# Kernel tuning notes

Hardware: AMD Instinct MI355X
Metric: run time of the kernel (lower is better)

## Reference

```python
import jax, jax.numpy as jnp
import numpy as np

EPS = 1e-5  # nn.RMSNorm eps


def setup_inputs() -> dict:
    key = jax.random.key(0)
    ks = jax.random.split(key, 8)
    B, L, D, R = 4, 4096, 2048, 4
    return {
        "h": jax.random.normal(ks[0], (B, L, D), jnp.float32),
        "h_o": jax.random.normal(ks[1], (B, L, D), jnp.float32),
        "static_alpha": jax.random.normal(ks[2], (R, R + 1), jnp.float32),
        "static_beta": jax.random.normal(ks[3], (R,), jnp.float32),
        "dynamic_alpha_fn": jax.random.normal(ks[4], (D, R + 1), jnp.float32) * 0.02,
        "dynamic_alpha_scale": jax.random.uniform(ks[5], (1,), jnp.float32, 0.005, 0.02),
        "dynamic_beta_fn": jax.random.normal(ks[6], (D,), jnp.float32) * 0.02,
        "dynamic_beta_scale": jnp.array([0.01], jnp.float32),
        "rms_weight": jax.random.uniform(ks[7], (D,), jnp.float32, 0.5, 1.5),
    }


def reference(h, h_o, static_alpha, static_beta, dynamic_alpha_fn,
              dynamic_alpha_scale, dynamic_beta_fn, dynamic_beta_scale,
              rms_weight):
    # RMSNorm over last dim with learnable weight (dynamic branch only)
    h_norm = h * jax.lax.rsqrt(jnp.mean(h * h, axis=-1, keepdims=True) + EPS) * rms_weight

    # dynamic alpha: [B,L,rate+1] offset broadcast against static [rate,rate+1]
    alpha_offset = jnp.tanh(h_norm @ dynamic_alpha_fn) * dynamic_alpha_scale  # [B,L,R+1]
    alpha = alpha_offset[:, :, None, :] + static_alpha                        # [B,L,R,R+1]

    # dynamic beta: scalar offset per token broadcast against static [rate]
    beta_offset = jnp.tanh(h_norm @ dynamic_beta_fn) * dynamic_beta_scale     # [B,L] * [1]
    beta = beta_offset[..., None] + static_beta                               # [B,L,R]

    # connect_width: mix_h[b,l,c,d] = sum_r alpha[b,l,r,c] * h[b,l,d]
    mix_h = jnp.einsum('blrc,bld->blcd', alpha, h)                            # [B,L,R+1,D]

    # connect_depth: broadcast outer product beta x h_o plus old streams, sum over rate
    out = jnp.sum(beta[..., None] * h_o[:, :, None, :] + mix_h[:, :, 1:, :], axis=2)
    return out  # [B,L,D]
```

## Files before the change

### kernel.cpp

```cpp
#include <hip/hip_runtime.h>
#include <math.h>


constexpr int D    = 2048;
constexpr int RATE = 4;
constexpr float EPS = 1e-5f;
constexpr int TPB  = 8;

__global__ __launch_bounds__(256) void hyperconn_kernel(
    const float* __restrict__ h,
    const float* __restrict__ h_o,
    const float* __restrict__ sa,
    const float* __restrict__ sb,
    const float* __restrict__ fa,
    const float* __restrict__ a_sc,
    const float* __restrict__ fb,
    const float* __restrict__ b_sc,
    const float* __restrict__ w,
    float* __restrict__ out)
{
    const int tid  = threadIdx.x;
    const int d0   = tid * 8;
    const int wave = tid >> 6;

    float4 wa = *reinterpret_cast<const float4*>(w + d0);
    float4 wb = *reinterpret_cast<const float4*>(w + d0 + 4);
    const float wv[8] = {wa.x, wa.y, wa.z, wa.w, wb.x, wb.y, wb.z, wb.w};

    float fav[32];
    {
        float tmp[40];
        #pragma unroll
        for (int q = 0; q < 10; ++q) {
            float4 t = *reinterpret_cast<const float4*>(fa + (size_t)d0 * 5 + q * 4);
            tmp[q*4+0]=t.x; tmp[q*4+1]=t.y; tmp[q*4+2]=t.z; tmp[q*4+3]=t.w;
        }
        #pragma unroll
        for (int j = 0; j < 8; ++j)
            #pragma unroll
            for (int c = 0; c < 4; ++c)
                fav[j*4+c] = tmp[j*5 + 1 + c];
    }
    float4 fba = *reinterpret_cast<const float4*>(fb + d0);
    float4 fbb = *reinterpret_cast<const float4*>(fb + d0 + 4);
    const float fbv[8] = {fba.x, fba.y, fba.z, fba.w, fbb.x, fbb.y, fbb.z, fbb.w};

    const float a4 = a_sc[0] * (float)RATE;
    const float b4 = b_sc[0] * (float)RATE;
    float cs = 0.f;
    #pragma unroll
    for (int r = 0; r < RATE; ++r)
        #pragma unroll
        for (int c = 1; c <= RATE; ++c)
            cs += sa[r * (RATE + 1) + c];
    const float sbsum = sb[0] + sb[1] + sb[2] + sb[3];

    __shared__ float red[2][4][6];

    const size_t t0 = (size_t)blockIdx.x * TPB;

    float4 hb0[2], hb1[2], ob0[2], ob1[2];
    {
        const size_t base = t0 * D + d0;
        hb0[0] = *reinterpret_cast<const float4*>(h   + base);
        hb1[0] = *reinterpret_cast<const float4*>(h   + base + 4);
        ob0[0] = *reinterpret_cast<const float4*>(h_o + base);
        ob1[0] = *reinterpret_cast<const float4*>(h_o + base + 4);
    }

    #pragma unroll
    for (int i = 0; i < TPB; ++i) {
        const int cur = i & 1;
        const int nxt = cur ^ 1;

        if (i + 1 < TPB) {
            const size_t nb = (t0 + i + 1) * D + d0;
            hb0[nxt] = *reinterpret_cast<const float4*>(h   + nb);
            hb1[nxt] = *reinterpret_cast<const float4*>(h   + nb + 4);
            ob0[nxt] = *reinterpret_cast<const float4*>(h_o + nb);
            ob1[nxt] = *reinterpret_cast<const float4*>(h_o + nb + 4);
        }

        const float hv[8] = {hb0[cur].x, hb0[cur].y, hb0[cur].z, hb0[cur].w,
                             hb1[cur].x, hb1[cur].y, hb1[cur].z, hb1[cur].w};

        float acc[6] = {0.f, 0.f, 0.f, 0.f, 0.f, 0.f};
        #pragma unroll
        for (int j = 0; j < 8; ++j) {
            const float x  = hv[j];
            const float xw = x * wv[j];
            acc[0] = fmaf(x,  x,          acc[0]);
            acc[1] = fmaf(xw, fav[j*4+0], acc[1]);
            acc[2] = fmaf(xw, fav[j*4+1], acc[2]);
            acc[3] = fmaf(xw, fav[j*4+2], acc[3]);
            acc[4] = fmaf(xw, fav[j*4+3], acc[4]);
            acc[5] = fmaf(xw, fbv[j],     acc[5]);
        }

        #pragma unroll
        for (int off = 32; off > 0; off >>= 1)
            #pragma unroll
            for (int k = 0; k < 6; ++k) acc[k] += __shfl_down(acc[k], off);

        if ((tid & 63) == 0) {
            #pragma unroll
            for (int k = 0; k < 6; ++k) red[cur][wave][k] = acc[k];
        }
        __syncthreads();
        float tot[6];
        #pragma unroll
        for (int k = 0; k < 6; ++k)
            tot[k] = red[cur][0][k] + red[cur][1][k] + red[cur][2][k] + red[cur][3][k];

        const float rms  = rsqrtf(tot[0] * (1.0f / (float)D) + EPS);
        const float s_h  = a4 * (tanhf(tot[1] * rms) + tanhf(tot[2] * rms) +
                                 tanhf(tot[3] * rms) + tanhf(tot[4] * rms)) + cs;
        const float s_ho = b4 * tanhf(tot[5] * rms) + sbsum;

        const size_t base = (t0 + i) * D + d0;
        float4 r0, r1;
        r0.x = fmaf(s_ho, ob0[cur].x, s_h * hv[0]);
        r0.y = fmaf(s_ho, ob0[cur].y, s_h * hv[1]);
        r0.z = fmaf(s_ho, ob0[cur].z, s_h * hv[2]);
        r0.w = fmaf(s_ho, ob0[cur].w, s_h * hv[3]);
        r1.x = fmaf(s_ho, ob1[cur].x, s_h * hv[4]);
        r1.y = fmaf(s_ho, ob1[cur].y, s_h * hv[5]);
        r1.z = fmaf(s_ho, ob1[cur].z, s_h * hv[6]);
        r1.w = fmaf(s_ho, ob1[cur].w, s_h * hv[7]);
        *reinterpret_cast<float4*>(out + base)     = r0;
        *reinterpret_cast<float4*>(out + base + 4) = r1;
    }
}

extern "C" void kernel_launch(void* const* d_in, const int* in_sizes, int n_in,
                              void* d_out, int out_size, void* d_ws, size_t ws_size,
                              hipStream_t stream) {
    const float* h    = (const float*)d_in[0];
    const float* h_o  = (const float*)d_in[1];
    const float* sa   = (const float*)d_in[2];
    const float* sb   = (const float*)d_in[3];
    const float* fa   = (const float*)d_in[4];
    const float* a_sc = (const float*)d_in[5];
    const float* fb   = (const float*)d_in[6];
    const float* b_sc = (const float*)d_in[7];
    const float* w    = (const float*)d_in[8];
    float* out = (float*)d_out;

    const int ntok   = in_sizes[0] / D;
    const int blocks = ntok / TPB;
    hyperconn_kernel<<<blocks, 256, 0, stream>>>(h, h_o, sa, sb, fa, a_sc, fb, b_sc, w, out);
}
```

Measured before the change: 84.19 us.

## Batch all token reductions behind one barrier and prefetch all h rows

Loads all eight token rows of h into registers up front, computes every token's partial reductions, and writes them to a per-token shared array. A single __syncthreads then replaces the per-token barriers, and h_o is loaded only in the epilogue. tanhf is replaced with an exp-based fast tanh. This is meant to cut barrier stalls and put more loads in flight, at the cost of higher register use (64 extra floats for h) and slightly lower tanh accuracy.

```diff
diff --git a/kernel.cpp b/kernel.cpp
--- a/kernel.cpp
+++ b/kernel.cpp
@@ -6,6 +6,11 @@
 constexpr int RATE = 4;
 constexpr float EPS = 1e-5f;
 constexpr int TPB  = 8;
+
+__device__ __forceinline__ float fast_tanh(float x) {
+    const float e = __expf(2.0f * x);
+    return 1.0f - 2.0f / (e + 1.0f);
+}
 
 __global__ __launch_bounds__(256) void hyperconn_kernel(
     const float* __restrict__ h,
@@ -22,6 +27,15 @@
     const int tid  = threadIdx.x;
     const int d0   = tid * 8;
     const int wave = tid >> 6;
+    const size_t t0 = (size_t)blockIdx.x * TPB;
+
+    float4 hA[TPB], hB[TPB];
+    #pragma unroll
+    for (int i = 0; i < TPB; ++i) {
+        const float* p = h + (t0 + i) * D + d0;
+        hA[i] = *reinterpret_cast<const float4*>(p);
+        hB[i] = *reinterpret_cast<const float4*>(p + 4);
+    }
 
     float4 wa = *reinterpret_cast<const float4*>(w + d0);
     float4 wb = *reinterpret_cast<const float4*>(w + d0 + 4);
@@ -55,35 +69,12 @@
             cs += sa[r * (RATE + 1) + c];
     const float sbsum = sb[0] + sb[1] + sb[2] + sb[3];
 
-    __shared__ float red[2][4][6];
-
-    const size_t t0 = (size_t)blockIdx.x * TPB;
-
-    float4 hb0[2], hb1[2], ob0[2], ob1[2];
-    {
-        const size_t base = t0 * D + d0;
-        hb0[0] = *reinterpret_cast<const float4*>(h   + base);
-        hb1[0] = *reinterpret_cast<const float4*>(h   + base + 4);
-        ob0[0] = *reinterpret_cast<const float4*>(h_o + base);
-        ob1[0] = *reinterpret_cast<const float4*>(h_o + base + 4);
-    }
+    alignas(16) __shared__ float red[TPB][24];
 
     #pragma unroll
     for (int i = 0; i < TPB; ++i) {
-        const int cur = i & 1;
-        const int nxt = cur ^ 1;
-
-        if (i + 1 < TPB) {
-            const size_t nb = (t0 + i + 1) * D + d0;
-            hb0[nxt] = *reinterpret_cast<const float4*>(h   + nb);
-            hb1[nxt] = *reinterpret_cast<const float4*>(h   + nb + 4);
-            ob0[nxt] = *reinterpret_cast<const float4*>(h_o + nb);
-            ob1[nxt] = *reinterpret_cast<const float4*>(h_o + nb + 4);
-        }
-
-        const float hv[8] = {hb0[cur].x, hb0[cur].y, hb0[cur].z, hb0[cur].w,
-                             hb1[cur].x, hb1[cur].y, hb1[cur].z, hb1[cur].w};
-
+        const float hv[8] = {hA[i].x, hA[i].y, hA[i].z, hA[i].w,
+                             hB[i].x, hB[i].y, hB[i].z, hB[i].w};
         float acc[6] = {0.f, 0.f, 0.f, 0.f, 0.f, 0.f};
         #pragma unroll
         for (int j = 0; j < 8; ++j) {
@@ -96,37 +87,51 @@
             acc[4] = fmaf(xw, fav[j*4+3], acc[4]);
             acc[5] = fmaf(xw, fbv[j],     acc[5]);
         }
-
         #pragma unroll
         for (int off = 32; off > 0; off >>= 1)
             #pragma unroll
             for (int k = 0; k < 6; ++k) acc[k] += __shfl_down(acc[k], off);
-
         if ((tid & 63) == 0) {
             #pragma unroll
-            for (int k = 0; k < 6; ++k) red[cur][wave][k] = acc[k];
+            for (int k = 0; k < 6; ++k) red[i][wave * 6 + k] = acc[k];
         }
-        __syncthreads();
-        float tot[6];
-        #pragma unroll
-        for (int k = 0; k < 6; ++k)
-            tot[k] = red[cur][0][k] + red[cur][1][k] + red[cur][2][k] + red[cur][3][k];
+    }
 
-        const float rms  = rsqrtf(tot[0] * (1.0f / (float)D) + EPS);
-        const float s_h  = a4 * (tanhf(tot[1] * rms) + tanhf(tot[2] * rms) +
-                                 tanhf(tot[3] * rms) + tanhf(tot[4] * rms)) + cs;
-        const float s_ho = b4 * tanhf(tot[5] * rms) + sbsum;
+    __syncthreads();
 
+    #pragma unroll
+    for (int i = 0; i < TPB; ++i) {
         const size_t base = (t0 + i) * D + d0;
+        const float4 oa = *reinterpret_cast<const float4*>(h_o + base);
+        const float4 ob = *reinterpret_cast<const float4*>(h_o + base + 4);
+
+        const float4 f0 = *reinterpret_cast<const float4*>(&red[i][0]);
+        const float4 f1 = *reinterpret_cast<const float4*>(&red[i][4]);
+        const float4 f2 = *reinterpret_cast<const float4*>(&red[i][8]);
+        const float4 f3 = *reinterpret_cast<const float4*>(&red[i][12]);
+        const float4 f4 = *reinterpret_cast<const float4*>(&red[i][16]);
+        const float4 f5 = *reinterpret_cast<const float4*>(&red[i][20]);
+        const float tot0 = f0.x + f1.z + f3.x + f4.z;
+        const float tot1 = f0.y + f1.w + f3.y + f4.w;
+        const float tot2 = f0.z + f2.x + f3.z + f5.x;
+        const float tot3 = f0.w + f2.y + f3.w + f5.y;
+        const float tot4 = f1.x + f2.z + f4.x + f5.z;
+        const float tot5 = f1.y + f2.w + f4.y + f5.w;
+
+        const float rms  = rsqrtf(tot0 * (1.0f / (float)D) + EPS);
+        const float s_h  = a4 * (fast_tanh(tot1 * rms) + fast_tanh(tot2 * rms) +
+                                 fast_tanh(tot3 * rms) + fast_tanh(tot4 * rms)) + cs;
+        const float s_ho = b4 * fast_tanh(tot5 * rms) + sbsum;
+
         float4 r0, r1;
-        r0.x = fmaf(s_ho, ob0[cur].x, s_h * hv[0]);
-        r0.y = fmaf(s_ho, ob0[cur].y, s_h * hv[1]);
-        r0.z = fmaf(s_ho, ob0[cur].z, s_h * hv[2]);
-        r0.w = fmaf(s_ho, ob0[cur].w, s_h * hv[3]);
-        r1.x = fmaf(s_ho, ob1[cur].x, s_h * hv[4]);
-        r1.y = fmaf(s_ho, ob1[cur].y, s_h * hv[5]);
-        r1.z = fmaf(s_ho, ob1[cur].z, s_h * hv[6]);
-        r1.w = fmaf(s_ho, ob1[cur].w, s_h * hv[7]);
+        r0.x = fmaf(s_ho, oa.x, s_h * hA[i].x);
+        r0.y = fmaf(s_ho, oa.y, s_h * hA[i].y);
+        r0.z = fmaf(s_ho, oa.z, s_h * hA[i].z);
+        r0.w = fmaf(s_ho, oa.w, s_h * hA[i].w);
+        r1.x = fmaf(s_ho, ob.x, s_h * hB[i].x);
+        r1.y = fmaf(s_ho, ob.y, s_h * hB[i].y);
+        r1.z = fmaf(s_ho, ob.z, s_h * hB[i].z);
+        r1.w = fmaf(s_ho, ob.w, s_h * hB[i].w);
         *reinterpret_cast<float4*>(out + base)     = r0;
         *reinterpret_cast<float4*>(out + base + 4) = r1;
     }
```

New measurement: 86.23 us (median of 5 runs). 2.4% more time.
